# Performance work log

Measured on AMD Instinct MI355X. Metric: run time of the kernel, lower is better.

The kernel has to match this reference:

```python
import jax, jax.numpy as jnp
import numpy as np

DIM = 256
HEADS = 8
WS = 7
MLP_HIDDEN = int(DIM * 2.0)
LN_EPS = 1e-5


def _ln(x, g, b):
    m = x.mean(-1, keepdims=True)
    v = ((x - m) ** 2).mean(-1, keepdims=True)
    return (x - m) / jnp.sqrt(v + LN_EPS) * g + b


def setup_inputs() -> dict:
    key = jax.random.key(0)
    ks = jax.random.split(key, 6)
    B, H, W, C = 32, 56, 56, DIM
    s = lambda k, shape: jax.random.normal(k, shape, jnp.float32) * 0.02
    return {
        "x": jax.random.normal(ks[0], (B, H * W, C), jnp.float32),
        "H": H,
        "W": W,
        "norm1_g": jnp.ones((C,), jnp.float32),
        "norm1_b": jnp.zeros((C,), jnp.float32),
        "in_proj_w": s(ks[1], (3 * C, C)),
        "in_proj_b": jnp.zeros((3 * C,), jnp.float32),
        "out_proj_w": s(ks[2], (C, C)),
        "out_proj_b": jnp.zeros((C,), jnp.float32),
        "norm2_g": jnp.ones((C,), jnp.float32),
        "norm2_b": jnp.zeros((C,), jnp.float32),
        "mlp_w1": s(ks[3], (MLP_HIDDEN, C)),
        "mlp_b1": jnp.zeros((MLP_HIDDEN,), jnp.float32),
        "mlp_w2": s(ks[4], (C, MLP_HIDDEN)),
        "mlp_b2": jnp.zeros((C,), jnp.float32),
    }


def reference(x, H, W, norm1_g, norm1_b, in_proj_w, in_proj_b, out_proj_w,
              out_proj_b, norm2_g, norm2_b, mlp_w1, mlp_b1, mlp_w2, mlp_b2):
    B, N, C = x.shape
    ws = WS
    shortcut = x

    h = _ln(x, norm1_g, norm1_b).reshape(B, H, W, C)  # channels-last (equiv. math)
    pad_h = (ws - H % ws) % ws
    pad_w = (ws - W % ws) % ws
    h = jnp.pad(h, ((0, 0), (0, pad_h), (0, pad_w), (0, 0)), mode="reflect")
    Hp, Wp = H + pad_h, W + pad_w
    nh, nw = Hp // ws, Wp // ws

    # window partition -> (B*nh*nw, ws*ws, C)
    h = h.reshape(B, nh, ws, nw, ws, C).transpose(0, 1, 3, 2, 4, 5)
    h = h.reshape(B * nh * nw, ws * ws, C)

    # torch nn.MultiheadAttention (batch_first), q=k=v=h
    hd = C // HEADS
    qkv = h @ in_proj_w.T + in_proj_b               # (Bw, L, 3C)
    q, k, v = jnp.split(qkv, 3, axis=-1)
    Bw, L, _ = q.shape
    q = q.reshape(Bw, L, HEADS, hd).transpose(0, 2, 1, 3)
    k = k.reshape(Bw, L, HEADS, hd).transpose(0, 2, 1, 3)
    v = v.reshape(Bw, L, HEADS, hd).transpose(0, 2, 1, 3)
    scores = jnp.einsum("bhqd,bhkd->bhqk", q, k) / jnp.sqrt(jnp.float32(hd))
    attn = jax.nn.softmax(scores, axis=-1)
    o = jnp.einsum("bhqk,bhkd->bhqd", attn, v)
    o = o.transpose(0, 2, 1, 3).reshape(Bw, L, C)
    o = o @ out_proj_w.T + out_proj_b

    # window merge, crop padding
    o = o.reshape(B, nh, nw, ws, ws, C).transpose(0, 1, 3, 2, 4, 5)
    o = o.reshape(B, Hp, Wp, C)[:, :H, :W, :].reshape(B, N, C)

    x = shortcut + o
    h2 = _ln(x, norm2_g, norm2_b)
    h2 = jax.nn.gelu(h2 @ mlp_w1.T + mlp_b1, approximate=False) @ mlp_w2.T + mlp_b2
    return x + h2
```

## Files before the change

### kernel.cpp

```cpp
#include <hip/hip_runtime.h>
#include <hip/hip_bf16.h>
#include <math.h>

#define NTOK 3136
#define C_ 256
#define HEADS_ 8
#define HD 32
#define WS_ 7
#define L_ 49
#define NWIN 2048
#define NWH 16384
#define M_ 100352
#define MLPH 512
#define WHSZ 2048

typedef __bf16 bf16x8 __attribute__((ext_vector_type(8)));
typedef float f32x4 __attribute__((ext_vector_type(4)));

__device__ __forceinline__ unsigned short f2bf(float f) {
    union { float f; unsigned u; } v; v.f = f;
    unsigned r = v.u + 0x7fffu + ((v.u >> 16) & 1u);
    return (unsigned short)(r >> 16);
}
__device__ __forceinline__ float bf2f(unsigned short s) {
    union { unsigned u; float f; } v; v.u = ((unsigned)s) << 16;
    return v.f;
}

__device__ __forceinline__ int t2rr(int t) {
    int win = t / L_;
    int l   = t - win * L_;
    int b_  = win >> 6, wh = (win >> 3) & 7, ww = win & 7;
    int ld7 = l / WS_;
    int y   = wh * WS_ + ld7;
    int xc  = ww * WS_ + (l - ld7 * WS_);
    return b_ * NTOK + y * 56 + xc;
}

template <int NBN>
__device__ __forceinline__ void xcd_decode(int nb, int& bm, int& bn) {
    int h = blockIdx.x;
    int fid = (h & 7) * (nb >> 3) + (h >> 3);
    int bmi = fid / NBN;
    bm = bmi * 128;
    bn = (fid - bmi * NBN) * 128;
}

__global__ __launch_bounds__(256) void cvt4_kernel(
    const float* __restrict__ a, const float* __restrict__ b,
    const float* __restrict__ c2, const float* __restrict__ d,
    unsigned short* __restrict__ out)
{
    int i = (blockIdx.x * 256 + threadIdx.x) * 4;
    const float* src; int off;
    if (i < 196608)      { src = a;  off = i; }
    else if (i < 262144) { src = b;  off = i - 196608; }
    else if (i < 393216) { src = c2; off = i - 262144; }
    else                 { src = d;  off = i - 393216; }
    float4 v = *(const float4*)(src + off);
    unsigned short o[4];
    o[0] = f2bf(v.x); o[1] = f2bf(v.y); o[2] = f2bf(v.z); o[3] = f2bf(v.w);
    *(uint2*)(out + i) = *(const uint2*)o;
}

__global__ __launch_bounds__(256) void ln_kernel(
    const float* __restrict__ x, const float* __restrict__ gamma,
    const float* __restrict__ beta, unsigned short* __restrict__ out)
{
    int wave = threadIdx.x >> 6;
    int lane = threadIdx.x & 63;
    int p = blockIdx.x * 4 + wave;
    const float* row = x + (size_t)p * C_;
    float4 v = *(const float4*)(row + lane * 4);
    float s  = v.x + v.y + v.z + v.w;
    float ss = v.x * v.x + v.y * v.y + v.z * v.z + v.w * v.w;
    #pragma unroll
    for (int m = 1; m < 64; m <<= 1) {
        s  += __shfl_xor(s, m, 64);
        ss += __shfl_xor(ss, m, 64);
    }
    float mean = s * (1.0f / C_);
    float var  = ss * (1.0f / C_) - mean * mean;
    float inv  = rsqrtf(var + 1e-5f);
    float4 gv = *(const float4*)(gamma + lane * 4);
    float4 bv = *(const float4*)(beta + lane * 4);
    int b_ = p / NTOK, n = p - b_ * NTOK;
    int y = n / 56, xc = n - y * 56;
    int win = (b_ * 8 + y / WS_) * 8 + xc / WS_;
    int l   = (y % WS_) * WS_ + (xc % WS_);
    size_t orow = (size_t)(win * L_ + l) * C_;
    unsigned short o[4];
    o[0] = f2bf((v.x - mean) * inv * gv.x + bv.x);
    o[1] = f2bf((v.y - mean) * inv * gv.y + bv.y);
    o[2] = f2bf((v.z - mean) * inv * gv.z + bv.z);
    o[3] = f2bf((v.w - mean) * inv * gv.w + bv.w);
    *(uint2*)(out + orow + lane * 4) = *(const uint2*)o;
}

#define GBK 64

__device__ __forceinline__ void gload_lds16(const void* g, void* l) {
    __builtin_amdgcn_global_load_lds(
        (const __attribute__((address_space(1))) unsigned*)g,
        (__attribute__((address_space(3))) unsigned*)l, 16, 0, 0);
}

__global__ __launch_bounds__(256) void mgemm_qkv(
    const unsigned short* __restrict__ A, const unsigned short* __restrict__ W,
    const float* __restrict__ bias, unsigned short* __restrict__ qkv)
{
    __shared__ __align__(16) unsigned short As[8192];
    __shared__ __align__(16) unsigned short Bs[8192];

    int tid  = threadIdx.x;
    int w    = tid >> 6;
    int lane = tid & 63;
    int wr = w >> 1, wc = w & 1;
    int bm, bn;
    xcd_decode<6>(gridDim.x, bm, bn);
    int srow8 = lane >> 3;
    int scol  = ((lane & 7) ^ srow8) * 8;
    int c = lane & 15, hi = lane >> 4;

    f32x4 acc[4][4] = {};

    for (int k0 = 0; k0 < 256; k0 += GBK) {
        #pragma unroll
        for (int it = 0; it < 4; ++it) {
            int rb = it * 32 + w * 8;
            gload_lds16(A + (size_t)(bm + rb + srow8) * 256 + k0 + scol, As + rb * 64);
            gload_lds16(W + (size_t)(bn + rb + srow8) * 256 + k0 + scol, Bs + rb * 64);
        }
        __syncthreads();
        #pragma unroll
        for (int kk = 0; kk < 2; ++kk) {
            bf16x8 af[4], bf[4];
            int hs = ((kk * 4 + hi) ^ (c & 7)) * 8;
            #pragma unroll
            for (int mi = 0; mi < 4; ++mi)
                af[mi] = *(const bf16x8*)&As[(wr * 64 + mi * 16 + c) * 64 + hs];
            #pragma unroll
            for (int ni = 0; ni < 4; ++ni)
                bf[ni] = *(const bf16x8*)&Bs[(wc * 64 + ni * 16 + c) * 64 + hs];
            #pragma unroll
            for (int mi = 0; mi < 4; ++mi)
                #pragma unroll
                for (int ni = 0; ni < 4; ++ni)
                    acc[mi][ni] = __builtin_amdgcn_mfma_f32_16x16x32_bf16(
                        af[mi], bf[ni], acc[mi][ni], 0, 0, 0);
        }
        __syncthreads();
    }

    #pragma unroll
    for (int mi = 0; mi < 4; ++mi) {
        #pragma unroll
        for (int r = 0; r < 4; ++r) {
            int row = bm + wr * 64 + mi * 16 + hi * 4 + r;
            int win = row / L_, l = row - win * L_;
            #pragma unroll
            for (int ni = 0; ni < 4; ++ni) {
                int col = bn + wc * 64 + ni * 16 + c;
                float val = acc[mi][ni][r] + bias[col];
                int which = col >> 8;
                int head  = (col >> 5) & 7;
                int d     = col & 31;
                int wh = win * HEADS_ + head;
                size_t base = (size_t)which * ((size_t)NWH * WHSZ) + (size_t)wh * WHSZ;
                size_t off;
                if (which == 2)
                    off = base + (size_t)(((l >> 3) * HD + d) << 3) + (l & 7);
                else
                    off = base + (size_t)l * HD + d;
                qkv[off] = f2bf(val);
            }
        }
    }
}

__global__ __launch_bounds__(256) void mattn(
    const unsigned short* __restrict__ qkv, unsigned short* __restrict__ o_win)
{
    __shared__ __align__(16) unsigned short P_lds[4][64][72];
    int wave = threadIdx.x >> 6, lane = threadIdx.x & 63;
    int c = lane & 15, hi = lane >> 4;
    int wh = blockIdx.x * 4 + wave;
    int win = wh >> 3, head = wh & 7;
    const unsigned short* qb = qkv + (size_t)wh * WHSZ;
    const unsigned short* kb = qb + (size_t)NWH * WHSZ;
    const unsigned short* vb = kb + (size_t)NWH * WHSZ;

    bf16x8 af[4], bk[4];
    #pragma unroll
    for (int mi = 0; mi < 4; ++mi)
        af[mi] = *(const bf16x8*)(qb + (mi * 16 + c) * HD + hi * 8);
    #pragma unroll
    for (int ni = 0; ni < 4; ++ni)
        bk[ni] = *(const bf16x8*)(kb + (ni * 16 + c) * HD + hi * 8);

    f32x4 sacc[4][4] = {};
    #pragma unroll
    for (int mi = 0; mi < 4; ++mi)
        #pragma unroll
        for (int ni = 0; ni < 4; ++ni)
            sacc[mi][ni] = __builtin_amdgcn_mfma_f32_16x16x32_bf16(
                af[mi], bk[ni], sacc[mi][ni], 0, 0, 0);

    const float scale = 0.17677669529663687f;
    float inv_[4][4];
    #pragma unroll
    for (int mi = 0; mi < 4; ++mi) {
        #pragma unroll
        for (int r = 0; r < 4; ++r) {
            float sv[4];
            float m = -1e30f;
            #pragma unroll
            for (int ni = 0; ni < 4; ++ni) {
                float v = sacc[mi][ni][r] * scale;
                v = (ni * 16 + c < L_) ? v : -1e30f;
                sv[ni] = v;
                m = fmaxf(m, v);
            }
            #pragma unroll
            for (int msk = 1; msk < 16; msk <<= 1)
                m = fmaxf(m, __shfl_xor(m, msk, 64));
            float sum = 0.f;
            unsigned short pb[4];
            #pragma unroll
            for (int ni = 0; ni < 4; ++ni) {
                float p = __expf(sv[ni] - m);
                sum += p;
                pb[ni] = f2bf(p);
            }
            #pragma unroll
            for (int msk = 1; msk < 16; msk <<= 1)
                sum += __shfl_xor(sum, msk, 64);
            inv_[mi][r] = 1.0f / sum;
            int q = mi * 16 + hi * 4 + r;
            #pragma unroll
            for (int ni = 0; ni < 4; ++ni)
                P_lds[wave][q][ni * 16 + c] = pb[ni];
        }
    }

    f32x4 oacc[4][2] = {};
    #pragma unroll
    for (int ks = 0; ks < 2; ++ks) {
        bf16x8 pa[4], bv[2];
        #pragma unroll
        for (int mi = 0; mi < 4; ++mi)
            pa[mi] = *(const bf16x8*)&P_lds[wave][mi * 16 + c][ks * 32 + hi * 8];
        #pragma unroll
        for (int ni = 0; ni < 2; ++ni)
            bv[ni] = *(const bf16x8*)(vb + ((ks * 4 + hi) * HD + ni * 16 + c) * 8);
        #pragma unroll
        for (int mi = 0; mi < 4; ++mi)
            #pragma unroll
            for (int ni = 0; ni < 2; ++ni)
                oacc[mi][ni] = __builtin_amdgcn_mfma_f32_16x16x32_bf16(
                    pa[mi], bv[ni], oacc[mi][ni], 0, 0, 0);
    }

    #pragma unroll
    for (int mi = 0; mi < 4; ++mi) {
        #pragma unroll
        for (int r = 0; r < 4; ++r) {
            int q = mi * 16 + hi * 4 + r;
            if (q < L_) {
                size_t rowoff = ((size_t)(win * L_ + q)) * C_ + head * HD;
                float iv = inv_[mi][r];
                #pragma unroll
                for (int ni = 0; ni < 2; ++ni)
                    o_win[rowoff + ni * 16 + c] = f2bf(oacc[mi][ni][r] * iv);
            }
        }
    }
}

#define XS 260

__global__ __launch_bounds__(512) void mgemm_ln(
    const unsigned short* __restrict__ A, const unsigned short* __restrict__ W,
    const float* __restrict__ bias, const float* __restrict__ x,
    const float* __restrict__ g2, const float* __restrict__ b2,
    unsigned short* __restrict__ x1_out, unsigned short* __restrict__ ln_out)
{
    __shared__ __align__(16) unsigned short pool[128 * XS];
    unsigned short* As = pool;
    unsigned short* Bs = pool + 8192;

    int tid  = threadIdx.x;
    int w    = tid >> 6;
    int lane = tid & 63;
    int wr = w >> 2, wc = w & 3;
    int bm = blockIdx.x * 128;
    int srow8 = lane >> 3;
    int scol  = ((lane & 7) ^ srow8) * 8;
    int c = lane & 15, hi = lane >> 4;

    f32x4 acc[4][4] = {};

    for (int k0 = 0; k0 < 256; k0 += GBK) {
        #pragma unroll
        for (int it = 0; it < 2; ++it) {
            int rb = it * 64 + w * 8;
            gload_lds16(A + (size_t)(bm + rb + srow8) * 256 + k0 + scol, As + rb * 64);
        }
        #pragma unroll
        for (int it = 0; it < 4; ++it) {
            int rb = it * 64 + w * 8;
            gload_lds16(W + (size_t)(rb + srow8) * 256 + k0 + scol, Bs + rb * 64);
        }
        __syncthreads();
        #pragma unroll
        for (int kk = 0; kk < 2; ++kk) {
            bf16x8 af[4], bf[4];
            int hs = ((kk * 4 + hi) ^ (c & 7)) * 8;
            #pragma unroll
            for (int mi = 0; mi < 4; ++mi)
                af[mi] = *(const bf16x8*)&As[(wr * 64 + mi * 16 + c) * 64 + hs];
            #pragma unroll
            for (int ni = 0; ni < 4; ++ni)
                bf[ni] = *(const bf16x8*)&Bs[(wc * 64 + ni * 16 + c) * 64 + hs];
            #pragma unroll
            for (int mi = 0; mi < 4; ++mi)
                #pragma unroll
                for (int ni = 0; ni < 4; ++ni)
                    acc[mi][ni] = __builtin_amdgcn_mfma_f32_16x16x32_bf16(
                        af[mi], bf[ni], acc[mi][ni], 0, 0, 0);
        }
        __syncthreads();
    }

    #pragma unroll
    for (int mi = 0; mi < 4; ++mi) {
        #pragma unroll
        for (int ni = 0; ni < 4; ++ni) {
            int colb = wc * 64 + ni * 16 + c;
            float bv = bias[colb];
            #pragma unroll
            for (int r = 0; r < 4; ++r)
                pool[(wr * 64 + mi * 16 + hi * 4 + r) * XS + colb] =
                    f2bf(acc[mi][ni][r] + bv);
        }
    }
    __syncthreads();

    float4 gv  = *(const float4*)(g2 + lane * 4);
    float4 bv2 = *(const float4*)(b2 + lane * 4);
    #pragma unroll 2
    for (int i = 0; i < 16; ++i) {
        int tl = w * 16 + i;
        int t = bm + tl;
        int rr = t2rr(t);
        float4 xv = *(const float4*)(x + (size_t)rr * C_ + lane * 4);
        uint2 ov = *(const uint2*)&pool[tl * XS + lane * 4];
        float x0 = xv.x + bf2f(ov.x & 0xffff);
        float x1 = xv.y + bf2f(ov.x >> 16);
        float x2 = xv.z + bf2f(ov.y & 0xffff);
        float x3 = xv.w + bf2f(ov.y >> 16);
        float s  = x0 + x1 + x2 + x3;
        float ss = x0 * x0 + x1 * x1 + x2 * x2 + x3 * x3;
        #pragma unroll
        for (int m = 1; m < 64; m <<= 1) {
            s  += __shfl_xor(s, m, 64);
            ss += __shfl_xor(ss, m, 64);
        }
        float mean = s * (1.0f / C_);
        float var  = ss * (1.0f / C_) - mean * mean;
        float inv  = rsqrtf(var + 1e-5f);
        uint2 xw, lw;
        xw.x = (unsigned)f2bf(x0) | ((unsigned)f2bf(x1) << 16);
        xw.y = (unsigned)f2bf(x2) | ((unsigned)f2bf(x3) << 16);
        float l0 = (x0 - mean) * inv * gv.x + bv2.x;
        float l1 = (x1 - mean) * inv * gv.y + bv2.y;
        float l2 = (x2 - mean) * inv * gv.z + bv2.z;
        float l3 = (x3 - mean) * inv * gv.w + bv2.w;
        lw.x = (unsigned)f2bf(l0) | ((unsigned)f2bf(l1) << 16);
        lw.y = (unsigned)f2bf(l2) | ((unsigned)f2bf(l3) << 16);
        *(uint2*)(x1_out + (size_t)t * C_ + lane * 4) = xw;
        *(uint2*)(ln_out + (size_t)t * C_ + lane * 4) = lw;
    }
}

#define TSS 136

__global__ __launch_bounds__(256) void mgemm_g(
    const unsigned short* __restrict__ A, const unsigned short* __restrict__ W,
    const float* __restrict__ bias, unsigned short* __restrict__ outp)
{
    __shared__ __align__(16) unsigned short pool[128 * TSS];
    unsigned short* As = pool;
    unsigned short* Bs = pool + 8192;
    unsigned short* Ts = pool;

    int tid  = threadIdx.x;
    int w    = tid >> 6;
    int lane = tid & 63;
    int wr = w >> 1, wc = w & 1;
    int bm, bn;
    xcd_decode<4>(gridDim.x, bm, bn);
    int srow8 = lane >> 3;
    int scol  = ((lane & 7) ^ srow8) * 8;
    int c = lane & 15, hi = lane >> 4;

    f32x4 acc[4][4] = {};

    for (int k0 = 0; k0 < 256; k0 += GBK) {
        #pragma unroll
        for (int it = 0; it < 4; ++it) {
            int rb = it * 32 + w * 8;
            gload_lds16(A + (size_t)(bm + rb + srow8) * 256 + k0 + scol, As + rb * 64);
            gload_lds16(W + (size_t)(bn + rb + srow8) * 256 + k0 + scol, Bs + rb * 64);
        }
        __syncthreads();
        #pragma unroll
        for (int kk = 0; kk < 2; ++kk) {
            bf16x8 af[4], bf[4];
            int hs = ((kk * 4 + hi) ^ (c & 7)) * 8;
            #pragma unroll
            for (int mi = 0; mi < 4; ++mi)
                af[mi] = *(const bf16x8*)&As[(wr * 64 + mi * 16 + c) * 64 + hs];
            #pragma unroll
            for (int ni = 0; ni < 4; ++ni)
                bf[ni] = *(const bf16x8*)&Bs[(wc * 64 + ni * 16 + c) * 64 + hs];
            #pragma unroll
            for (int mi = 0; mi < 4; ++mi)
                #pragma unroll
                for (int ni = 0; ni < 4; ++ni)
                    acc[mi][ni] = __builtin_amdgcn_mfma_f32_16x16x32_bf16(
                        af[mi], bf[ni], acc[mi][ni], 0, 0, 0);
        }
        __syncthreads();
    }

    #pragma unroll
    for (int mi = 0; mi < 4; ++mi) {
        #pragma unroll
        for (int ni = 0; ni < 4; ++ni) {
            int colb = wc * 64 + ni * 16 + c;
            float bv = bias[bn + colb];
            #pragma unroll
            for (int r = 0; r < 4; ++r) {
                float v = acc[mi][ni][r] + bv;
                float a = 1.5957691216f * (v + 0.044715f * v * v * v);
                float g = v / (1.0f + __expf(-a));
                Ts[(wr * 64 + mi * 16 + hi * 4 + r) * TSS + colb] = f2bf(g);
            }
        }
    }
    __syncthreads();

    #pragma unroll
    for (int it = 0; it < 8; ++it) {
        int id = it * 256 + tid;
        int row = id >> 4, cx = (id & 15) * 8;
        uint4 v = *(const uint4*)&Ts[row * TSS + cx];
        *(uint4*)&outp[(size_t)(bm + row) * MLPH + bn + cx] = v;
    }
}

__global__ __launch_bounds__(256) void mgemm_out(
    const unsigned short* __restrict__ A, const unsigned short* __restrict__ W,
    const float* __restrict__ bias, const unsigned short* __restrict__ x1,
    float* __restrict__ dout)
{
    __shared__ __align__(16) unsigned short pool[16896];
    unsigned short* As = pool;
    unsigned short* Bs = pool + 8192;
    float* stg = (float*)pool;

    int tid  = threadIdx.x;
    int w    = tid >> 6;
    int lane = tid & 63;
    int wr = w >> 1, wc = w & 1;
    int bm, bn;
    xcd_decode<2>(gridDim.x, bm, bn);
    int srow8 = lane >> 3;
    int scol  = ((lane & 7) ^ srow8) * 8;
    int c = lane & 15, hi = lane >> 4;

    f32x4 acc[4][4] = {};

    for (int k0 = 0; k0 < 512; k0 += GBK) {
        #pragma unroll
        for (int it = 0; it < 4; ++it) {
            int rb = it * 32 + w * 8;
            gload_lds16(A + (size_t)(bm + rb + srow8) * 512 + k0 + scol, As + rb * 64);
            gload_lds16(W + (size_t)(bn + rb + srow8) * 512 + k0 + scol, Bs + rb * 64);
        }
        __syncthreads();
        #pragma unroll
        for (int kk = 0; kk < 2; ++kk) {
            bf16x8 af[4], bf[4];
            int hs = ((kk * 4 + hi) ^ (c & 7)) * 8;
            #pragma unroll
            for (int mi = 0; mi < 4; ++mi)
                af[mi] = *(const bf16x8*)&As[(wr * 64 + mi * 16 + c) * 64 + hs];
            #pragma unroll
            for (int ni = 0; ni < 4; ++ni)
                bf[ni] = *(const bf16x8*)&Bs[(wc * 64 + ni * 16 + c) * 64 + hs];
            #pragma unroll
            for (int mi = 0; mi < 4; ++mi)
                #pragma unroll
                for (int ni = 0; ni < 4; ++ni)
                    acc[mi][ni] = __builtin_amdgcn_mfma_f32_16x16x32_bf16(
                        af[mi], bf[ni], acc[mi][ni], 0, 0, 0);
        }
        __syncthreads();
    }

    #pragma unroll
    for (int p = 0; p < 2; ++p) {
        if (wr == p) {
            #pragma unroll
            for (int mi = 0; mi < 4; ++mi)
                #pragma unroll
                for (int ni = 0; ni < 4; ++ni) {
                    int colb = wc * 64 + ni * 16 + c;
                    float bv = bias[bn + colb];
                    #pragma unroll
                    for (int r = 0; r < 4; ++r)
                        stg[(mi * 16 + hi * 4 + r) * 132 + colb] =
                            acc[mi][ni][r] + bv;
                }
        }
        __syncthreads();
        #pragma unroll
        for (int i = 0; i < 8; ++i) {
            int lr = i * 8 + (tid >> 5);
            int t = bm + p * 64 + lr;
            int rr = t2rr(t);
            int col4 = (tid & 31) * 4;
            float4 v = *(const float4*)&stg[lr * 132 + col4];
            uint2 rv = *(const uint2*)&x1[(size_t)t * C_ + bn + col4];
            v.x += bf2f(rv.x & 0xffff);
            v.y += bf2f(rv.x >> 16);
            v.z += bf2f(rv.y & 0xffff);
            v.w += bf2f(rv.y >> 16);
            *(float4*)&dout[(size_t)rr * C_ + bn + col4] = v;
        }
        __syncthreads();
    }
}

extern "C" void kernel_launch(void* const* d_in, const int* in_sizes, int n_in,
                              void* d_out, int out_size, void* d_ws, size_t ws_size,
                              hipStream_t stream)
{
    (void)in_sizes; (void)n_in; (void)out_size; (void)ws_size;
    const float* x    = (const float*)d_in[0];
    const float* n1g  = (const float*)d_in[3];
    const float* n1b  = (const float*)d_in[4];
    const float* wqkv = (const float*)d_in[5];
    const float* bqkv = (const float*)d_in[6];
    const float* wout = (const float*)d_in[7];
    const float* bout = (const float*)d_in[8];
    const float* n2g  = (const float*)d_in[9];
    const float* n2b  = (const float*)d_in[10];
    const float* w1   = (const float*)d_in[11];
    const float* b1   = (const float*)d_in[12];
    const float* w2   = (const float*)d_in[13];
    const float* b2   = (const float*)d_in[14];
    float* out = (float*)d_out;

    unsigned short* bufA_bf = (unsigned short*)d_ws;
    unsigned short* qkv_bf  = bufA_bf + (size_t)M_ * C_;
    unsigned short* x1_bf   = qkv_bf + (size_t)3 * NWH * WHSZ;
    unsigned short* ln2_bf  = x1_bf + (size_t)M_ * C_;
    unsigned short* wqkv_bf = ln2_bf + (size_t)M_ * C_;
    unsigned short* wout_bf = wqkv_bf + 768 * 256;
    unsigned short* w1_bf   = wout_bf + 256 * 256;
    unsigned short* w2_bf   = w1_bf + 512 * 256;
    unsigned short* gelu    = qkv_bf;

    cvt4_kernel<<<512, 256, 0, stream>>>(wqkv, wout, w1, w2, wqkv_bf);

    ln_kernel<<<M_ / 4, 256, 0, stream>>>(x, n1g, n1b, bufA_bf);

    mgemm_qkv<<<(M_ / 128) * 6, 256, 0, stream>>>(
        bufA_bf, wqkv_bf, bqkv, qkv_bf);

    mattn<<<NWH / 4, 256, 0, stream>>>(qkv_bf, bufA_bf);

    mgemm_ln<<<M_ / 128, 512, 0, stream>>>(
        bufA_bf, wout_bf, bout, x, n2g, n2b, x1_bf, ln2_bf);

    mgemm_g<<<(M_ / 128) * 4, 256, 0, stream>>>(ln2_bf, w1_bf, b1, gelu);

    mgemm_out<<<(M_ / 128) * 2, 256, 0, stream>>>(gelu, w2_bf, b2, x1_bf, out);
}
```

Before: 382.0 us.

## Stage QKV epilogue through LDS for vector stores and store V row-major

The QKV GEMM epilogue now writes bias-added bf16 results into a padded shared-memory tile, then each thread issues 16-byte coalesced stores into per-window-head planes, replacing scattered 2-byte stores. V is now kept in the same row-major layout as Q and K, and the attention kernel loads each V tile into LDS and builds the transposed MFMA operands from there. This trades extra LDS traffic, a barrier and strided LDS reads for much better global write coalescing in the GEMM.

Measured after the change: 370.9 us. 1.03x faster.

```diff
diff --git a/kernel.cpp b/kernel.cpp
--- a/kernel.cpp
+++ b/kernel.cpp
@@ -105,12 +105,16 @@
         (__attribute__((address_space(3))) unsigned*)l, 16, 0, 0);
 }
 
+#define TSS 136
+
 __global__ __launch_bounds__(256) void mgemm_qkv(
     const unsigned short* __restrict__ A, const unsigned short* __restrict__ W,
     const float* __restrict__ bias, unsigned short* __restrict__ qkv)
 {
-    __shared__ __align__(16) unsigned short As[8192];
-    __shared__ __align__(16) unsigned short Bs[8192];
+    __shared__ __align__(16) unsigned short pool[128 * TSS];
+    unsigned short* As = pool;
+    unsigned short* Bs = pool + 8192;
+    unsigned short* Ts = pool;
 
     int tid  = threadIdx.x;
     int w    = tid >> 6;
@@ -155,26 +159,30 @@
     #pragma unroll
     for (int mi = 0; mi < 4; ++mi) {
         #pragma unroll
-        for (int r = 0; r < 4; ++r) {
-            int row = bm + wr * 64 + mi * 16 + hi * 4 + r;
-            int win = row / L_, l = row - win * L_;
-            #pragma unroll
-            for (int ni = 0; ni < 4; ++ni) {
-                int col = bn + wc * 64 + ni * 16 + c;
-                float val = acc[mi][ni][r] + bias[col];
-                int which = col >> 8;
-                int head  = (col >> 5) & 7;
-                int d     = col & 31;
-                int wh = win * HEADS_ + head;
-                size_t base = (size_t)which * ((size_t)NWH * WHSZ) + (size_t)wh * WHSZ;
-                size_t off;
-                if (which == 2)
-                    off = base + (size_t)(((l >> 3) * HD + d) << 3) + (l & 7);
-                else
-                    off = base + (size_t)l * HD + d;
-                qkv[off] = f2bf(val);
-            }
-        }
+        for (int ni = 0; ni < 4; ++ni) {
+            int colb = wc * 64 + ni * 16 + c;
+            float bv = bias[bn + colb];
+            #pragma unroll
+            for (int r = 0; r < 4; ++r)
+                Ts[(wr * 64 + mi * 16 + hi * 4 + r) * TSS + colb] =
+                    f2bf(acc[mi][ni][r] + bv);
+        }
+    }
+    __syncthreads();
+
+    int which  = bn >> 8;
+    int bn_off = bn & 255;
+    unsigned short* plane = qkv + (size_t)which * ((size_t)NWH * WHSZ);
+    #pragma unroll
+    for (int it = 0; it < 8; ++it) {
+        int id = it * 256 + tid;
+        int row = id >> 4, cx = (id & 15) * 8;
+        int grow = bm + row;
+        int win = grow / L_, l = grow - win * L_;
+        int col = bn_off + cx;
+        int head = col >> 5, d0 = col & 31;
+        uint4 v = *(const uint4*)&Ts[row * TSS + cx];
+        *(uint4*)&plane[(size_t)(win * HEADS_ + head) * WHSZ + l * HD + d0] = v;
     }
 }
 
@@ -190,6 +198,13 @@
     const unsigned short* kb = qb + (size_t)NWH * WHSZ;
     const unsigned short* vb = kb + (size_t)NWH * WHSZ;
 
+    unsigned short* Vs = &P_lds[wave][0][0];
+    #pragma unroll
+    for (int i = 0; i < 4; ++i) {
+        int idx = i * 64 + lane;
+        *(uint4*)&Vs[idx * 8] = *(const uint4*)(vb + idx * 8);
+    }
+
     bf16x8 af[4], bk[4];
     #pragma unroll
     for (int mi = 0; mi < 4; ++mi)
@@ -197,6 +212,18 @@
     #pragma unroll
     for (int ni = 0; ni < 4; ++ni)
         bk[ni] = *(const bf16x8*)(kb + (ni * 16 + c) * HD + hi * 8);
+
+    bf16x8 vf[2][2];
+    #pragma unroll
+    for (int ks = 0; ks < 2; ++ks)
+        #pragma unroll
+        for (int ni = 0; ni < 2; ++ni) {
+            union { unsigned short s[8]; bf16x8 v; } uu;
+            #pragma unroll
+            for (int j = 0; j < 8; ++j)
+                uu.s[j] = Vs[(ks * 32 + hi * 8 + j) * HD + ni * 16 + c];
+            vf[ks][ni] = uu.v;
+        }
 
     f32x4 sacc[4][4] = {};
     #pragma unroll
@@ -246,19 +273,16 @@
     f32x4 oacc[4][2] = {};
     #pragma unroll
     for (int ks = 0; ks < 2; ++ks) {
-        bf16x8 pa[4], bv[2];
+        bf16x8 pa[4];
         #pragma unroll
         for (int mi = 0; mi < 4; ++mi)
             pa[mi] = *(const bf16x8*)&P_lds[wave][mi * 16 + c][ks * 32 + hi * 8];
         #pragma unroll
-        for (int ni = 0; ni < 2; ++ni)
-            bv[ni] = *(const bf16x8*)(vb + ((ks * 4 + hi) * HD + ni * 16 + c) * 8);
-        #pragma unroll
         for (int mi = 0; mi < 4; ++mi)
             #pragma unroll
             for (int ni = 0; ni < 2; ++ni)
                 oacc[mi][ni] = __builtin_amdgcn_mfma_f32_16x16x32_bf16(
-                    pa[mi], bv[ni], oacc[mi][ni], 0, 0, 0);
+                    pa[mi], vf[ks][ni], oacc[mi][ni], 0, 0, 0);
     }
 
     #pragma unroll
@@ -383,8 +407,6 @@
     }
 }
 
-#define TSS 136
-
 __global__ __launch_bounds__(256) void mgemm_g(
     const unsigned short* __restrict__ A, const unsigned short* __restrict__ W,
     const float* __restrict__ bias, unsigned short* __restrict__ outp)
```
